# Kernel tuning notes

Hardware: AMD Instinct MI355X
Metric: run time of the kernel (lower is better)

The kernel has to match this reference:

```python
import jax, jax.numpy as jnp
import numpy as np

B, T, C = 4, 2048, 1024
H = 16
HD = C // H  # 64
OBS_DIM, ACT_DIM = 17, 6
JOINED_DIM = OBS_DIM + ACT_DIM + 2  # 25


def _make_mask():
    # tril causal mask with every (JOINED_DIM-1 + k*JOINED_DIM)-th column zeroed (RL branch)
    m = np.tril(np.ones((T, T), dtype=np.float32))
    m[:, JOINED_DIM - 1::JOINED_DIM] = 0.0
    return jnp.asarray(m > 0)  # bool [T, T]


MASK = _make_mask()


def setup_inputs() -> dict:
    key = jax.random.key(0)
    ks = jax.random.split(key, 9)
    s = 1.0 / np.sqrt(C)
    return {
        "x": jax.random.normal(ks[0], (B, T, C), dtype=jnp.float32),
        "Wq": jax.random.normal(ks[1], (C, C), dtype=jnp.float32) * s,
        "bq": jax.random.normal(ks[2], (C,), dtype=jnp.float32) * s,
        "Wk": jax.random.normal(ks[3], (C, C), dtype=jnp.float32) * s,
        "bk": jax.random.normal(ks[4], (C,), dtype=jnp.float32) * s,
        "Wv": jax.random.normal(ks[5], (C, C), dtype=jnp.float32) * s,
        "bv": jax.random.normal(ks[6], (C,), dtype=jnp.float32) * s,
        "Wp": jax.random.normal(ks[7], (C, C), dtype=jnp.float32) * s,
        "bp": jax.random.normal(ks[8], (C,), dtype=jnp.float32) * s,
    }


def reference(x, Wq, bq, Wk, bk, Wv, bv, Wp, bp):
    # torch nn.Linear: y = x @ W.T + b
    def split_heads(t):  # [B,T,C] -> [B,H,T,HD]
        return t.reshape(B, T, H, HD).transpose(0, 2, 1, 3)

    q = split_heads(x @ Wq.T + bq)
    k = split_heads(x @ Wk.T + bk)
    v = split_heads(x @ Wv.T + bv)

    att = jnp.einsum("bhqd,bhkd->bhqk", q, k) * (1.0 / np.sqrt(HD))
    att = jnp.where(MASK[None, None, :, :], att, -jnp.inf)
    att = jax.nn.softmax(att, axis=-1)
    # dropout layers are identity in eval mode

    y = jnp.einsum("bhqk,bhkd->bhqd", att, v)  # [B,H,T,HD]
    y = y.transpose(0, 2, 1, 3).reshape(B, T, C)
    return y @ Wp.T + bp
```

## Files before the change

kernel.cpp:

```cpp
#include <hip/hip_runtime.h>
#include <hip/hip_bf16.h>


typedef __attribute__((ext_vector_type(8))) short short8;
typedef __attribute__((ext_vector_type(4))) float floatx4;
typedef unsigned short us;

__device__ __forceinline__ us f2bf(float f){
    union { __hip_bfloat16 h; us u; } cv;
    cv.h = __float2bfloat16(f);
    return cv.u;
}

__device__ __forceinline__ void ld_g2l16(const void* g, void* l){
    __builtin_amdgcn_global_load_lds((const __attribute__((address_space(1))) void*)g,
                                     (__attribute__((address_space(3))) void*)l, 16, 0, 0);
}

__global__ __launch_bounds__(256) void cvt_kernel(const float* __restrict__ in,
                                                  us* __restrict__ out, int n4){
    int i = blockIdx.x * 256 + threadIdx.x;
    if (i < n4){
        float4 v = reinterpret_cast<const float4*>(in)[i];
        ushort4 o;
        o.x = f2bf(v.x); o.y = f2bf(v.y); o.z = f2bf(v.z); o.w = f2bf(v.w);
        reinterpret_cast<ushort4*>(out)[i] = o;
    }
}

__global__ __launch_bounds__(256) void cvt4_kernel(const float* __restrict__ w0, const float* __restrict__ w1,
                                                   const float* __restrict__ w2, const float* __restrict__ w3,
                                                   us* __restrict__ o0, us* __restrict__ o1,
                                                   us* __restrict__ o2, us* __restrict__ o3){
    int wsel = blockIdx.x >> 10;
    int i = (blockIdx.x & 1023) * 256 + threadIdx.x;
    const float* src = (wsel == 0) ? w0 : (wsel == 1) ? w1 : (wsel == 2) ? w2 : w3;
    us* dst = (wsel == 0) ? o0 : (wsel == 1) ? o1 : (wsel == 2) ? o2 : o3;
    float4 v = reinterpret_cast<const float4*>(src)[i];
    ushort4 o;
    o.x = f2bf(v.x); o.y = f2bf(v.y); o.z = f2bf(v.z); o.w = f2bf(v.w);
    reinterpret_cast<ushort4*>(dst)[i] = o;
}


#define QSCALE 0.1803368801111244f

#define BAR() __builtin_amdgcn_s_barrier()
#define LGKM0() do { asm volatile("s_waitcnt lgkmcnt(0)" ::: "memory"); __builtin_amdgcn_sched_barrier(0); } while(0)
#define VMC2() asm volatile("s_waitcnt vmcnt(2)" ::: "memory")
#define VMC0() asm volatile("s_waitcnt vmcnt(0)" ::: "memory")

#define STAGE_A8(buf, half, kt) do { \
    _Pragma("unroll") \
    for (int i_ = 0; i_ < 2; i_++) \
        ld_g2l16(A + (size_t)(m0 + (half)*128 + srow[i_])*1024 + (kt)*64 + sgr[i_]*8, \
                 &smem[(buf)*16384 + (half)*8192 + (i_*8 + wave)*512]); \
} while(0)

#define STAGE_B8(buf, half, kt) do { \
    _Pragma("unroll") \
    for (int i_ = 0; i_ < 2; i_++) \
        ld_g2l16(Wb + (size_t)(n0 + (half)*128 + srow[i_])*1024 + (kt)*64 + sgr[i_]*8, \
                 &smem[32768 + (buf)*16384 + (half)*8192 + (i_*8 + wave)*512]); \
} while(0)

#define LOAD_AF8(buf, IH) do { \
    _Pragma("unroll") \
    for (int i_ = 0; i_ < 4; i_++){ \
        int ra_ = wm*128 + (IH)*64 + i_*16 + lane15; \
        _Pragma("unroll") \
        for (int ks_ = 0; ks_ < 2; ks_++){ \
            int ga_ = (ks_*4 + quad) ^ (ra_ & 7); \
            af[i_][ks_] = *reinterpret_cast<const short8*>(&smem[(buf)*16384 + ra_*64 + ga_*8]); \
        } } \
} while(0)

#define LOAD_BF8(buf, JH) do { \
    _Pragma("unroll") \
    for (int j_ = 0; j_ < 2; j_++){ \
        int rb_ = wn*64 + (JH)*32 + j_*16 + lane15; \
        _Pragma("unroll") \
        for (int ks_ = 0; ks_ < 2; ks_++){ \
            int gb_ = (ks_*4 + quad) ^ (rb_ & 7); \
            bf[JH][j_][ks_] = *reinterpret_cast<const short8*>(&smem[32768 + (buf)*16384 + rb_*64 + gb_*8]); \
        } } \
} while(0)

#define MFMA_Q8(IH, JH) do { \
    __builtin_amdgcn_s_setprio(1); \
    _Pragma("unroll") \
    for (int ks_ = 0; ks_ < 2; ks_++) \
        _Pragma("unroll") \
        for (int i_ = 0; i_ < 4; i_++) \
            _Pragma("unroll") \
            for (int j_ = 0; j_ < 2; j_++) \
                acc[(IH)*4 + i_][(JH)*2 + j_] = __builtin_amdgcn_mfma_f32_16x16x32_bf16( \
                    af[i_][ks_], bf[JH][j_][ks_], acc[(IH)*4 + i_][(JH)*2 + j_], 0, 0, 0); \
    __builtin_amdgcn_s_setprio(0); \
} while(0)

__global__ __launch_bounds__(512, 2) void gemm_qkv8(
    const us* __restrict__ A,
    const us* __restrict__ Wqb, const us* __restrict__ Wkb, const us* __restrict__ Wvb,
    const float* __restrict__ bq, const float* __restrict__ bk, const float* __restrict__ bv,
    us* __restrict__ qo, us* __restrict__ ko, us* __restrict__ vto)
{
    __shared__ us smem[65536];
    const int tid = threadIdx.x;
    const int lane = tid & 63;
    const int wave = tid >> 6;
    const int lane15 = lane & 15;
    const int quad = lane >> 4;
    const int wm = wave >> 2;
    const int wn = wave & 3;
    const int seg = blockIdx.x >> 2;
    const int n0 = (blockIdx.x & 3) * 256;
    const int m0 = blockIdx.y * 256;

    const us* Wb = (seg == 0) ? Wqb : (seg == 1) ? Wkb : Wvb;
    const float* bias = (seg == 0) ? bq : (seg == 1) ? bk : bv;

    int srow[2], sgr[2];
    #pragma unroll
    for (int i = 0; i < 2; i++){
        int s = (i*8 + wave)*64 + lane;
        srow[i] = s >> 3;
        sgr[i] = (s & 7) ^ ((s >> 3) & 7);
    }

    floatx4 zero = {0.f, 0.f, 0.f, 0.f};
    floatx4 acc[8][4];
    #pragma unroll
    for (int i = 0; i < 8; i++)
        #pragma unroll
        for (int j = 0; j < 4; j++) acc[i][j] = zero;
    short8 af[4][2];
    short8 bf[2][2][2];

    STAGE_A8(0, 0, 0); STAGE_A8(0, 1, 0); STAGE_B8(0, 0, 0); STAGE_B8(0, 1, 0);
    STAGE_A8(1, 0, 1);
    VMC2(); BAR();

    #pragma unroll 1
    for (int it = 0; it < 8; it++){
        const int t = 2*it;
        LOAD_AF8(0, 0); LOAD_BF8(0, 0);
        STAGE_A8(1, 1, t+1);
        BAR(); LGKM0();
        MFMA_Q8(0, 0);
        BAR();
        LOAD_BF8(0, 1);
        STAGE_B8(1, 0, t+1);
        BAR(); LGKM0();
        MFMA_Q8(0, 1);
        BAR();
        LOAD_AF8(0, 1);
        STAGE_B8(1, 1, t+1);
        BAR(); LGKM0();
        MFMA_Q8(1, 1);
        BAR();
        if (it < 7) STAGE_A8(0, 0, t+2);
        BAR(); LGKM0();
        MFMA_Q8(1, 0);
        if (it < 7) { VMC2(); } else { VMC0(); }
        BAR();
        LOAD_AF8(1, 0); LOAD_BF8(1, 0);
        if (it < 7) STAGE_A8(0, 1, t+2);
        BAR(); LGKM0();
        MFMA_Q8(0, 0);
        BAR();
        LOAD_BF8(1, 1);
        if (it < 7) STAGE_B8(0, 0, t+2);
        BAR(); LGKM0();
        MFMA_Q8(0, 1);
        BAR();
        LOAD_AF8(1, 1);
        if (it < 7) STAGE_B8(0, 1, t+2);
        BAR(); LGKM0();
        MFMA_Q8(1, 1);
        BAR();
        if (it < 7) STAGE_A8(1, 0, t+3);
        BAR(); LGKM0();
        MFMA_Q8(1, 0);
        if (it < 7) { VMC2(); } else { VMC0(); }
        BAR();
    }

    if (seg < 2){
        #pragma unroll
        for (int i = 0; i < 8; i++){
            #pragma unroll
            for (int j = 0; j < 4; j++){
                int n = n0 + wn*64 + j*16 + lane15;
                float bvv = bias[n];
                #pragma unroll
                for (int r = 0; r < 4; r++){
                    int m = m0 + wm*128 + i*16 + quad*4 + r;
                    float val = acc[i][j][r] + bvv;
                    if (seg == 0){
                        qo[(size_t)m*1024 + n] = f2bf(val * QSCALE);
                    } else {
                        int b = m >> 11, tt = m & 2047;
                        int h = n >> 6,  d = n & 63;
                        ko[(((size_t)b*16 + h)*2048 + tt)*64 + d] = f2bf(val);
                    }
                }
            }
        }
    } else {
        us* lCT = smem;
        const int b = m0 >> 11;
        const int t0 = m0 & 2047;
        #pragma unroll
        for (int p = 0; p < 2; p++){
            if (p) __syncthreads();
            if (wm == p){
                #pragma unroll
                for (int j = 0; j < 4; j++){
                    int nl = wn*64 + j*16 + lane15;
                    float bvv = bias[n0 + nl];
                    #pragma unroll
                    for (int i = 0; i < 8; i++){
                        int ml = i*16 + quad*4;
                        unsigned int lo = (unsigned int)f2bf(acc[i][j][0] + bvv) |
                                          ((unsigned int)f2bf(acc[i][j][1] + bvv) << 16);
                        unsigned int hi = (unsigned int)f2bf(acc[i][j][2] + bvv) |
                                          ((unsigned int)f2bf(acc[i][j][3] + bvv) << 16);
                        uint2 pk2; pk2.x = lo; pk2.y = hi;
                        *reinterpret_cast<uint2*>(&lCT[(size_t)nl*136 + ml]) = pk2;
                    }
                }
            }
            __syncthreads();
            int nl = tid >> 1;
            int half = tid & 1;
            int nC = n0 + nl;
            int h = nC >> 6, d = nC & 63;
            us* dst = vto + (((size_t)b*16 + h)*64 + d)*2048 + t0 + p*128 + half*64;
            #pragma unroll
            for (int ii = 0; ii < 8; ii++){
                uint4 v = *reinterpret_cast<const uint4*>(&lCT[(size_t)nl*136 + half*64 + ii*8]);
                *reinterpret_cast<uint4*>(dst + ii*8) = v;
            }
        }
    }
}

__device__ __forceinline__ void pstore_rg(
    floatx4 (&s)[4], us* pw, bool diag, int rgrow, int j0, int jr, const int (&res)[4],
    int lane15, int quad)
{
    #pragma unroll
    for (int tj = 0; tj < 4; tj++){
        bool bad = (res[tj] + jr) == 24;
        #pragma unroll
        for (int r = 0; r < 4; r++){
            float p = __builtin_amdgcn_exp2f(s[tj][r]);
            bool kill = bad || (diag && (j0 + tj*16 + lane15 > rgrow + quad*4 + r));
            pw[(quad*4 + r)*72 + tj*16 + lane15] = f2bf(kill ? 0.f : p);
        }
    }
}

__global__ __launch_bounds__(256, 3) void flash_attn(
    const us* __restrict__ q,
    const us* __restrict__ k,
    const us* __restrict__ vT,
    us* __restrict__ y)
{
    __shared__ us lK[2][64*64];
    __shared__ us lV[2][64*64];
    __shared__ us lP[4][2][16*72];
    const int tid = threadIdx.x;
    const int lane = tid & 63;
    const int wave = tid >> 6;
    const int lane15 = lane & 15;
    const int quad = lane >> 4;
    const int lin = blockIdx.x;
    const int qt2 = 15 - (lin >> 6);
    const int bh = lin & 63;
    const int b = bh >> 4, h = bh & 15;
    const int rg0 = qt2*128 + wave*16;
    const int rg1 = rg0 + 64;
    const int nIter = 2*qt2 + 2;

    const us* kb = k  + (size_t)bh*2048*64;
    const us* vb = vT + (size_t)bh*64*2048;

    const us* q0 = q + ((size_t)b*2048 + rg0 + lane15)*1024 + h*64 + quad*8;
    const us* q1 = q + ((size_t)b*2048 + rg1 + lane15)*1024 + h*64 + quad*8;
    short8 qf0a = *reinterpret_cast<const short8*>(q0);
    short8 qf0b = *reinterpret_cast<const short8*>(q0 + 32);
    short8 qf1a = *reinterpret_cast<const short8*>(q1);
    short8 qf1b = *reinterpret_cast<const short8*>(q1 + 32);

    floatx4 zero = {0.f, 0.f, 0.f, 0.f};
    floatx4 acc0[4], acc1[4];
    #pragma unroll
    for (int d = 0; d < 4; d++){ acc0[d] = zero; acc1[d] = zero; }
    floatx4 lacc0 = zero, lacc1 = zero;

    us* pw0 = &lP[wave][0][0];
    us* pw1 = &lP[wave][1][0];

    short8 onesb;
    #pragma unroll
    for (int e = 0; e < 8; e++) onesb[e] = (short)0x3F80;

    int res[4];
    #pragma unroll
    for (int tj = 0; tj < 4; tj++) res[tj] = (tj*16 + lane15) % 25;
    int jr = 0;

    int srow[2], sgr[2];
    #pragma unroll
    for (int i = 0; i < 2; i++){
        int s = (i*4 + wave)*64 + lane;
        srow[i] = s >> 3;
        sgr[i] = (s & 7) ^ ((s >> 3) & 7);
    }

    #pragma unroll
    for (int i = 0; i < 2; i++){
        ld_g2l16(kb + (size_t)srow[i]*64 + sgr[i]*8, &lK[0][(i*4 + wave)*512]);
        ld_g2l16(vb + (size_t)srow[i]*2048 + sgr[i]*8, &lV[0][(i*4 + wave)*512]);
    }

    for (int it = 0; it < nIter; it++){
        const int j0 = it*64;
        __syncthreads();

        if (it + 1 < nIter){
            #pragma unroll
            for (int i = 0; i < 2; i++){
                ld_g2l16(kb + (size_t)(j0 + 64 + srow[i])*64 + sgr[i]*8,
                         &lK[(it + 1) & 1][(i*4 + wave)*512]);
                ld_g2l16(vb + (size_t)srow[i]*2048 + j0 + 64 + sgr[i]*8,
                         &lV[(it + 1) & 1][(i*4 + wave)*512]);
            }
        }

        const us* Kb = lK[it & 1];
        const us* Vb = lV[it & 1];
        const bool act0  = (it + 1 < nIter);
        const bool diag0 = (it + 2 == nIter);
        const bool diag1 = (it + 1 == nIter);

        floatx4 s0[4], s1[4];
        #pragma unroll
        for (int tj = 0; tj < 4; tj++){
            int rk = tj*16 + lane15;
            short8 kf0 = *reinterpret_cast<const short8*>(&Kb[rk*64 + ((quad     ^ (rk & 7)))*8]);
            short8 kf1 = *reinterpret_cast<const short8*>(&Kb[rk*64 + (((4+quad) ^ (rk & 7)))*8]);
            floatx4 z1 = __builtin_amdgcn_mfma_f32_16x16x32_bf16(qf1a, kf0, zero, 0, 0, 0);
            s1[tj]     = __builtin_amdgcn_mfma_f32_16x16x32_bf16(qf1b, kf1, z1,   0, 0, 0);
            if (act0){
                floatx4 z0 = __builtin_amdgcn_mfma_f32_16x16x32_bf16(qf0a, kf0, zero, 0, 0, 0);
                s0[tj]     = __builtin_amdgcn_mfma_f32_16x16x32_bf16(qf0b, kf1, z0,   0, 0, 0);
            }
        }

        pstore_rg(s1, pw1, diag1, rg1, j0, jr, res, lane15, quad);
        if (act0)
            pstore_rg(s0, pw0, diag0, rg0, j0, jr, res, lane15, quad);

        #pragma unroll
        for (int ks = 0; ks < 2; ks++){
            short8 pf1 = *reinterpret_cast<const short8*>(&pw1[lane15*72 + ks*32 + quad*8]);
            short8 pf0 = *reinterpret_cast<const short8*>(&pw0[lane15*72 + ks*32 + quad*8]);
            lacc1 = __builtin_amdgcn_mfma_f32_16x16x32_bf16(pf1, onesb, lacc1, 0, 0, 0);
            if (act0) lacc0 = __builtin_amdgcn_mfma_f32_16x16x32_bf16(pf0, onesb, lacc0, 0, 0, 0);
            #pragma unroll
            for (int dt = 0; dt < 4; dt++){
                int rv = dt*16 + lane15;
                short8 vf = *reinterpret_cast<const short8*>(&Vb[rv*64 + (((ks*4+quad) ^ (rv & 7)))*8]);
                acc1[dt] = __builtin_amdgcn_mfma_f32_16x16x32_bf16(pf1, vf, acc1[dt], 0, 0, 0);
                if (act0) acc0[dt] = __builtin_amdgcn_mfma_f32_16x16x32_bf16(pf0, vf, acc0[dt], 0, 0, 0);
            }
        }

        jr += 14; if (jr >= 25) jr -= 25;
    }

    float rl0[4], rl1[4];
    #pragma unroll
    for (int r = 0; r < 4; r++){ rl0[r] = 1.0f / lacc0[r]; rl1[r] = 1.0f / lacc1[r]; }
    #pragma unroll
    for (int dt = 0; dt < 4; dt++){
        #pragma unroll
        for (int r = 0; r < 4; r++){
            int t0 = rg0 + quad*4 + r;
            int t1 = rg1 + quad*4 + r;
            int cc = h*64 + dt*16 + lane15;
            y[((size_t)b*2048 + t0)*1024 + cc] = f2bf(acc0[dt][r] * rl0[r]);
            y[((size_t)b*2048 + t1)*1024 + cc] = f2bf(acc1[dt][r] * rl1[r]);
        }
    }
}

__global__ __launch_bounds__(256) void gemm_out(
    const us* __restrict__ A,
    const us* __restrict__ Wb,
    const float* __restrict__ bias,
    float* __restrict__ out)
{
    __shared__ us lA[128*64];
    __shared__ us lB[128*64];
    const int tid = threadIdx.x;
    const int lane = tid & 63;
    const int wave = tid >> 6;
    const int lane15 = lane & 15;
    const int quad = lane >> 4;
    const int wm = wave >> 1, wn = wave & 1;
    const int m0 = blockIdx.y * 128;
    const int n0 = blockIdx.x * 128;

    floatx4 zero = {0.f, 0.f, 0.f, 0.f};
    floatx4 acc[4][4];
    #pragma unroll
    for (int i = 0; i < 4; i++)
        #pragma unroll
        for (int j = 0; j < 4; j++) acc[i][j] = zero;

    int srow[4], sg[4];
    #pragma unroll
    for (int t = 0; t < 4; t++){
        int s = (t*4 + wave)*64 + lane;
        srow[t] = s >> 3;
        sg[t] = (s & 7) ^ ((s >> 3) & 7);
    }

    for (int k0 = 0; k0 < 1024; k0 += 64){
        #pragma unroll
        for (int t = 0; t < 4; t++){
            int chunk = t*4 + wave;
            ld_g2l16(A  + (size_t)(m0 + srow[t])*1024 + k0 + sg[t]*8, &lA[chunk*512]);
            ld_g2l16(Wb + (size_t)(n0 + srow[t])*1024 + k0 + sg[t]*8, &lB[chunk*512]);
        }
        __syncthreads();
        #pragma unroll
        for (int ks = 0; ks < 2; ks++){
            short8 af[4], bf[4];
            #pragma unroll
            for (int i = 0; i < 4; i++){
                int ra = wm*64 + i*16 + lane15;
                int ga = (ks*4 + quad) ^ (ra & 7);
                af[i] = *reinterpret_cast<const short8*>(&lA[ra*64 + ga*8]);
                int rb = wn*64 + i*16 + lane15;
                int gb = (ks*4 + quad) ^ (rb & 7);
                bf[i] = *reinterpret_cast<const short8*>(&lB[rb*64 + gb*8]);
            }
            #pragma unroll
            for (int i = 0; i < 4; i++)
                #pragma unroll
                for (int j = 0; j < 4; j++)
                    acc[i][j] = __builtin_amdgcn_mfma_f32_16x16x32_bf16(af[i], bf[j], acc[i][j], 0, 0, 0);
        }
        __syncthreads();
    }

    #pragma unroll
    for (int i = 0; i < 4; i++){
        #pragma unroll
        for (int j = 0; j < 4; j++){
            int n = n0 + wn*64 + j*16 + lane15;
            float bvv = bias[n];
            #pragma unroll
            for (int r = 0; r < 4; r++){
                int m = m0 + wm*64 + i*16 + quad*4 + r;
                out[(size_t)m*1024 + n] = acc[i][j][r] + bvv;
            }
        }
    }
}

extern "C" void kernel_launch(void* const* d_in, const int* in_sizes, int n_in,
                              void* d_out, int out_size, void* d_ws, size_t ws_size,
                              hipStream_t stream)
{
    const float* x  = (const float*)d_in[0];
    const float* Wq = (const float*)d_in[1];
    const float* bq = (const float*)d_in[2];
    const float* Wk = (const float*)d_in[3];
    const float* bk = (const float*)d_in[4];
    const float* Wv = (const float*)d_in[5];
    const float* bv = (const float*)d_in[6];
    const float* Wp = (const float*)d_in[7];
    const float* bp = (const float*)d_in[8];
    float* out = (float*)d_out;

    us* ws  = (us*)d_ws;
    us* xbf = ws;
    us* wqb = xbf + (size_t)8192*1024;
    us* wkb = wqb + (size_t)1024*1024;
    us* wvb = wkb + (size_t)1024*1024;
    us* wpb = wvb + (size_t)1024*1024;
    us* qws = wpb + (size_t)1024*1024;
    us* kws = qws + (size_t)8388608;
    us* vtw = kws + (size_t)8388608;
    us* yws = vtw + (size_t)8388608;

    cvt_kernel<<<8192, 256, 0, stream>>>(x, xbf, 2097152);
    cvt4_kernel<<<4096, 256, 0, stream>>>(Wq, Wk, Wv, Wp, wqb, wkb, wvb, wpb);

    gemm_qkv8<<<dim3(12, 32), 512, 0, stream>>>(xbf, wqb, wkb, wvb, bq, bk, bv, qws, kws, vtw);

    flash_attn<<<1024, 256, 0, stream>>>(qws, kws, vtw, yws);

    gemm_out<<<dim3(8, 64), 256, 0, stream>>>(yws, wpb, bp, out);
}
```

Before: 266.3 us.

## Shrink QKV GEMM tile to 256x128 with triple-buffered LDS pipeline

The QKV projection GEMM moves from 256x256 tiles with an 8-phase double-buffered schedule to 256x128 tiles with a 3-stage LDS ring buffer and two prefetched k-steps in flight. The grid doubles to 768 blocks, which is meant to improve CU occupancy and load balance on the device, and the schedule now has fewer barriers per k-step. In exchange, A-tile reuse per block halves, so more global/L2 traffic is spent on x, and LDS use grows to 144KB per block, which may limit residency to one block per CU. The V-transpose epilogue is simplified into a single pass over a 256-wide LDS staging buffer.

```diff
diff --git a/kernel.cpp b/kernel.cpp
--- a/kernel.cpp
+++ b/kernel.cpp
@@ -47,46 +47,46 @@
 
 #define BAR() __builtin_amdgcn_s_barrier()
 #define LGKM0() do { asm volatile("s_waitcnt lgkmcnt(0)" ::: "memory"); __builtin_amdgcn_sched_barrier(0); } while(0)
-#define VMC2() asm volatile("s_waitcnt vmcnt(2)" ::: "memory")
+#define VMC6() asm volatile("s_waitcnt vmcnt(6)" ::: "memory")
 #define VMC0() asm volatile("s_waitcnt vmcnt(0)" ::: "memory")
 
-#define STAGE_A8(buf, half, kt) do { \
+#define STAGE_A3(buf, kt) do { \
     _Pragma("unroll") \
-    for (int i_ = 0; i_ < 2; i_++) \
-        ld_g2l16(A + (size_t)(m0 + (half)*128 + srow[i_])*1024 + (kt)*64 + sgr[i_]*8, \
-                 &smem[(buf)*16384 + (half)*8192 + (i_*8 + wave)*512]); \
+    for (int c_ = 0; c_ < 4; c_++) \
+        ld_g2l16(A + (size_t)(m0 + srow[c_])*1024 + (kt)*64 + sgr[c_]*8, \
+                 &smem[(buf)*24576 + (c_*8 + wave)*512]); \
 } while(0)
 
-#define STAGE_B8(buf, half, kt) do { \
+#define STAGE_B3(buf, kt) do { \
     _Pragma("unroll") \
-    for (int i_ = 0; i_ < 2; i_++) \
-        ld_g2l16(Wb + (size_t)(n0 + (half)*128 + srow[i_])*1024 + (kt)*64 + sgr[i_]*8, \
-                 &smem[32768 + (buf)*16384 + (half)*8192 + (i_*8 + wave)*512]); \
+    for (int c_ = 0; c_ < 2; c_++) \
+        ld_g2l16(Wb + (size_t)(n0 + srow[c_])*1024 + (kt)*64 + sgr[c_]*8, \
+                 &smem[(buf)*24576 + 16384 + (c_*8 + wave)*512]); \
 } while(0)
 
-#define LOAD_AF8(buf, IH) do { \
+#define LOAD_AF3(buf, IH) do { \
     _Pragma("unroll") \
     for (int i_ = 0; i_ < 4; i_++){ \
         int ra_ = wm*128 + (IH)*64 + i_*16 + lane15; \
         _Pragma("unroll") \
         for (int ks_ = 0; ks_ < 2; ks_++){ \
             int ga_ = (ks_*4 + quad) ^ (ra_ & 7); \
-            af[i_][ks_] = *reinterpret_cast<const short8*>(&smem[(buf)*16384 + ra_*64 + ga_*8]); \
+            af[i_][ks_] = *reinterpret_cast<const short8*>(&smem[(buf)*24576 + ra_*64 + ga_*8]); \
         } } \
 } while(0)
 
-#define LOAD_BF8(buf, JH) do { \
+#define LOAD_BF3(buf) do { \
     _Pragma("unroll") \
     for (int j_ = 0; j_ < 2; j_++){ \
-        int rb_ = wn*64 + (JH)*32 + j_*16 + lane15; \
+        int rb_ = wn*32 + j_*16 + lane15; \
         _Pragma("unroll") \
         for (int ks_ = 0; ks_ < 2; ks_++){ \
             int gb_ = (ks_*4 + quad) ^ (rb_ & 7); \
-            bf[JH][j_][ks_] = *reinterpret_cast<const short8*>(&smem[32768 + (buf)*16384 + rb_*64 + gb_*8]); \
+            bf[j_][ks_] = *reinterpret_cast<const short8*>(&smem[(buf)*24576 + 16384 + rb_*64 + gb_*8]); \
         } } \
 } while(0)
 
-#define MFMA_Q8(IH, JH) do { \
+#define MFMA_PH3(IH) do { \
     __builtin_amdgcn_s_setprio(1); \
     _Pragma("unroll") \
     for (int ks_ = 0; ks_ < 2; ks_++) \
@@ -94,18 +94,18 @@
         for (int i_ = 0; i_ < 4; i_++) \
             _Pragma("unroll") \
             for (int j_ = 0; j_ < 2; j_++) \
-                acc[(IH)*4 + i_][(JH)*2 + j_] = __builtin_amdgcn_mfma_f32_16x16x32_bf16( \
-                    af[i_][ks_], bf[JH][j_][ks_], acc[(IH)*4 + i_][(JH)*2 + j_], 0, 0, 0); \
+                acc[(IH)*4 + i_][j_] = __builtin_amdgcn_mfma_f32_16x16x32_bf16( \
+                    af[i_][ks_], bf[j_][ks_], acc[(IH)*4 + i_][j_], 0, 0, 0); \
     __builtin_amdgcn_s_setprio(0); \
 } while(0)
 
-__global__ __launch_bounds__(512, 2) void gemm_qkv8(
+__global__ __launch_bounds__(512, 2) void gemm_qkv3(
     const us* __restrict__ A,
     const us* __restrict__ Wqb, const us* __restrict__ Wkb, const us* __restrict__ Wvb,
     const float* __restrict__ bq, const float* __restrict__ bk, const float* __restrict__ bv,
     us* __restrict__ qo, us* __restrict__ ko, us* __restrict__ vto)
 {
-    __shared__ us smem[65536];
+    __shared__ us smem[73728];
     const int tid = threadIdx.x;
     const int lane = tid & 63;
     const int wave = tid >> 6;
@@ -113,85 +113,56 @@
     const int quad = lane >> 4;
     const int wm = wave >> 2;
     const int wn = wave & 3;
-    const int seg = blockIdx.x >> 2;
-    const int n0 = (blockIdx.x & 3) * 256;
+    const int seg = blockIdx.x >> 3;
+    const int n0 = (blockIdx.x & 7) * 128;
     const int m0 = blockIdx.y * 256;
 
     const us* Wb = (seg == 0) ? Wqb : (seg == 1) ? Wkb : Wvb;
     const float* bias = (seg == 0) ? bq : (seg == 1) ? bk : bv;
 
-    int srow[2], sgr[2];
-    #pragma unroll
-    for (int i = 0; i < 2; i++){
-        int s = (i*8 + wave)*64 + lane;
-        srow[i] = s >> 3;
-        sgr[i] = (s & 7) ^ ((s >> 3) & 7);
+    int srow[4], sgr[4];
+    #pragma unroll
+    for (int c = 0; c < 4; c++){
+        int s = (c*8 + wave)*64 + lane;
+        srow[c] = s >> 3;
+        sgr[c] = (s & 7) ^ ((s >> 3) & 7);
     }
 
     floatx4 zero = {0.f, 0.f, 0.f, 0.f};
-    floatx4 acc[8][4];
+    floatx4 acc[8][2];
     #pragma unroll
     for (int i = 0; i < 8; i++)
         #pragma unroll
-        for (int j = 0; j < 4; j++) acc[i][j] = zero;
+        for (int j = 0; j < 2; j++) acc[i][j] = zero;
     short8 af[4][2];
-    short8 bf[2][2][2];
-
-    STAGE_A8(0, 0, 0); STAGE_A8(0, 1, 0); STAGE_B8(0, 0, 0); STAGE_B8(0, 1, 0);
-    STAGE_A8(1, 0, 1);
-    VMC2(); BAR();
-
-    #pragma unroll 1
-    for (int it = 0; it < 8; it++){
-        const int t = 2*it;
-        LOAD_AF8(0, 0); LOAD_BF8(0, 0);
-        STAGE_A8(1, 1, t+1);
+    short8 bf[2][2];
+
+    STAGE_A3(0, 0); STAGE_B3(0, 0);
+    STAGE_A3(1, 1); STAGE_B3(1, 1);
+    VMC6(); BAR();
+
+    #pragma unroll
+    for (int t = 0; t < 16; t++){
+        const int cur = t % 3, nxt = (t + 2) % 3;
+        LOAD_AF3(cur, 0); LOAD_BF3(cur);
+        if (t < 14) STAGE_A3(nxt, t + 2);
         BAR(); LGKM0();
-        MFMA_Q8(0, 0);
+        MFMA_PH3(0);
         BAR();
-        LOAD_BF8(0, 1);
-        STAGE_B8(1, 0, t+1);
+        LOAD_AF3(cur, 1);
+        if (t < 14) STAGE_B3(nxt, t + 2);
         BAR(); LGKM0();
-        MFMA_Q8(0, 1);
+        MFMA_PH3(1);
+        if (t < 14) { VMC6(); } else { VMC0(); }
         BAR();
-        LOAD_AF8(0, 1);
-        STAGE_B8(1, 1, t+1);
-        BAR(); LGKM0();
-        MFMA_Q8(1, 1);
-        BAR();
-        if (it < 7) STAGE_A8(0, 0, t+2);
-        BAR(); LGKM0();
-        MFMA_Q8(1, 0);
-        if (it < 7) { VMC2(); } else { VMC0(); }
-        BAR();
-        LOAD_AF8(1, 0); LOAD_BF8(1, 0);
-        if (it < 7) STAGE_A8(0, 1, t+2);
-        BAR(); LGKM0();
-        MFMA_Q8(0, 0);
-        BAR();
-        LOAD_BF8(1, 1);
-        if (it < 7) STAGE_B8(0, 0, t+2);
-        BAR(); LGKM0();
-        MFMA_Q8(0, 1);
-        BAR();
-        LOAD_AF8(1, 1);
-        if (it < 7) STAGE_B8(0, 1, t+2);
-        BAR(); LGKM0();
-        MFMA_Q8(1, 1);
-        BAR();
-        if (it < 7) STAGE_A8(1, 0, t+3);
-        BAR(); LGKM0();
-        MFMA_Q8(1, 0);
-        if (it < 7) { VMC2(); } else { VMC0(); }
-        BAR();
     }
 
     if (seg < 2){
         #pragma unroll
         for (int i = 0; i < 8; i++){
             #pragma unroll
-            for (int j = 0; j < 4; j++){
-                int n = n0 + wn*64 + j*16 + lane15;
+            for (int j = 0; j < 2; j++){
+                int n = n0 + wn*32 + j*16 + lane15;
                 float bvv = bias[n];
                 #pragma unroll
                 for (int r = 0; r < 4; r++){
@@ -212,36 +183,30 @@
         const int b = m0 >> 11;
         const int t0 = m0 & 2047;
         #pragma unroll
-        for (int p = 0; p < 2; p++){
-            if (p) __syncthreads();
-            if (wm == p){
-                #pragma unroll
-                for (int j = 0; j < 4; j++){
-                    int nl = wn*64 + j*16 + lane15;
-                    float bvv = bias[n0 + nl];
-                    #pragma unroll
-                    for (int i = 0; i < 8; i++){
-                        int ml = i*16 + quad*4;
-                        unsigned int lo = (unsigned int)f2bf(acc[i][j][0] + bvv) |
-                                          ((unsigned int)f2bf(acc[i][j][1] + bvv) << 16);
-                        unsigned int hi = (unsigned int)f2bf(acc[i][j][2] + bvv) |
-                                          ((unsigned int)f2bf(acc[i][j][3] + bvv) << 16);
-                        uint2 pk2; pk2.x = lo; pk2.y = hi;
-                        *reinterpret_cast<uint2*>(&lCT[(size_t)nl*136 + ml]) = pk2;
-                    }
-                }
-            }
-            __syncthreads();
-            int nl = tid >> 1;
-            int half = tid & 1;
-            int nC = n0 + nl;
-            int h = nC >> 6, d = nC & 63;
-            us* dst = vto + (((size_t)b*16 + h)*64 + d)*2048 + t0 + p*128 + half*64;
-            #pragma unroll
-            for (int ii = 0; ii < 8; ii++){
-                uint4 v = *reinterpret_cast<const uint4*>(&lCT[(size_t)nl*136 + half*64 + ii*8]);
-                *reinterpret_cast<uint4*>(dst + ii*8) = v;
-            }
+        for (int j = 0; j < 2; j++){
+            int nl = wn*32 + j*16 + lane15;
+            float bvv = bias[n0 + nl];
+            #pragma unroll
+            for (int i = 0; i < 8; i++){
+                int ml = wm*128 + i*16 + quad*4;
+                unsigned int lo = (unsigned int)f2bf(acc[i][j][0] + bvv) |
+                                  ((unsigned int)f2bf(acc[i][j][1] + bvv) << 16);
+                unsigned int hi = (unsigned int)f2bf(acc[i][j][2] + bvv) |
+                                  ((unsigned int)f2bf(acc[i][j][3] + bvv) << 16);
+                uint2 pk2; pk2.x = lo; pk2.y = hi;
+                *reinterpret_cast<uint2*>(&lCT[(size_t)nl*264 + ml]) = pk2;
+            }
+        }
+        __syncthreads();
+        int nl = tid >> 2;
+        int c4 = tid & 3;
+        int nC = n0 + nl;
+        int h = nC >> 6, d = nC & 63;
+        us* dst = vto + (((size_t)b*16 + h)*64 + d)*2048 + t0 + c4*64;
+        #pragma unroll
+        for (int ii = 0; ii < 8; ii++){
+            uint4 v = *reinterpret_cast<const uint4*>(&lCT[(size_t)nl*264 + c4*64 + ii*8]);
+            *reinterpret_cast<uint4*>(dst + ii*8) = v;
         }
     }
 }
@@ -503,7 +468,7 @@
     cvt_kernel<<<8192, 256, 0, stream>>>(x, xbf, 2097152);
     cvt4_kernel<<<4096, 256, 0, stream>>>(Wq, Wk, Wv, Wp, wqb, wkb, wvb, wpb);
 
-    gemm_qkv8<<<dim3(12, 32), 512, 0, stream>>>(xbf, wqb, wkb, wvb, bq, bk, bv, qws, kws, vtw);
+    gemm_qkv3<<<dim3(24, 32), 512, 0, stream>>>(xbf, wqb, wkb, wvb, bq, bk, bv, qws, kws, vtw);
 
     flash_attn<<<1024, 256, 0, stream>>>(qws, kws, vtw, yws);
 
```

After: 263.3 us. About the same (-1.1%).
